# Performance work log

Hardware: AMD Instinct MI355X
Metric: run time of the kernel (lower is better)

The kernel has to match this reference:

```python
import jax, jax.numpy as jnp
import numpy as np

B, S, D, H, N, E = 4, 2048, 512, 8, 1024, 16384


def setup_inputs() -> dict:
    key = jax.random.key(0)
    ks = jax.random.split(key, 16)
    rn = lambda k, shp, s=0.02: jax.random.normal(k, shp, jnp.float32) * s
    x = jax.random.normal(ks[0], (B, S, D), jnp.float32)
    edge_index = jax.random.randint(ks[1], (2, E), 0, N)
    # unique sorted node positions per batch (equivalent to node_mask with N ones)
    node_indices = jnp.sort(
        jax.vmap(lambda k: jax.random.permutation(k, S)[:N])(jax.random.split(ks[2], B)),
        axis=1,
    )
    z = lambda shp: jnp.zeros(shp, jnp.float32)
    o = lambda shp: jnp.ones(shp, jnp.float32)
    return {
        "x": x,
        "edge_index": edge_index,
        "node_indices": node_indices,
        "Wq": rn(ks[3], (D, D)), "bq": z((D,)),
        "Wk": rn(ks[4], (D, D)), "bk": z((D,)),
        "Wv": rn(ks[5], (D, D)), "bv": z((D,)),
        "Wo": rn(ks[6], (D, D)), "bo": z((D,)),
        "Wf1": rn(ks[7], (D, 4 * D)), "bf1": z((4 * D,)),
        "Wf2": rn(ks[8], (4 * D, D)), "bf2": z((D,)),
        "g1": o((D,)), "be1": z((D,)),
        "g2": o((D,)), "be2": z((D,)),
        "g3": o((D,)), "be3": z((D,)),
        "Wg": rn(ks[9], (2 * D, D)), "bg": z((D,)),
        "Wgs": rn(ks[10], (D, D)), "Wgn": rn(ks[11], (D, D)), "bgn": z((D,)),
    }


def _ln(t, g, b, eps=1e-5):
    m = t.mean(-1, keepdims=True)
    v = ((t - m) ** 2).mean(-1, keepdims=True)
    return (t - m) * jax.lax.rsqrt(v + eps) * g + b


def reference(x, edge_index, node_indices, Wq, bq, Wk, bk, Wv, bv, Wo, bo,
              Wf1, bf1, Wf2, bf2, g1, be1, g2, be2, g3, be3, Wg, bg,
              Wgs, Wgn, bgn):
    Bs, Ss, Ds = x.shape
    Hn = H
    hd = Ds // Hn
    Nn = node_indices.shape[1]

    # --- self-attention (pre-norm, residual; dropout = eval identity) ---
    nx = _ln(x, g1, be1)
    q = (nx @ Wq + bq).reshape(Bs, Ss, Hn, hd).transpose(0, 2, 1, 3)
    k = (nx @ Wk + bk).reshape(Bs, Ss, Hn, hd).transpose(0, 2, 1, 3)
    v = (nx @ Wv + bv).reshape(Bs, Ss, Hn, hd).transpose(0, 2, 1, 3)
    scores = jnp.einsum('bhqd,bhkd->bhqk', q, k) / jnp.sqrt(jnp.float32(hd))
    attn = jax.nn.softmax(scores, axis=-1)
    ao = jnp.einsum('bhqk,bhkd->bhqd', attn, v).transpose(0, 2, 1, 3).reshape(Bs, Ss, Ds)
    x = x + ao @ Wo + bo

    # --- gather -> GNN -> scatter with sigmoid gate fusion ---
    nx2 = _ln(x, g2, be2)
    bidx = jnp.arange(Bs)[:, None]
    nodes = nx2[bidx, node_indices]                       # [B, N, D] gather
    src, dst = edge_index[0], edge_index[1]
    msgs = nodes[:, src, :]                               # [B, E, D]
    agg = jax.vmap(lambda m: jax.ops.segment_sum(m, dst, num_segments=Nn))(msgs)
    upd = jax.nn.relu(nodes @ Wgs + agg @ Wgn + bgn)      # GCN-like update
    gnn_out = jnp.zeros_like(nx2).at[bidx, node_indices].set(upd)  # scatter-back
    gate = jax.nn.sigmoid(jnp.concatenate([nx2, gnn_out], axis=-1) @ Wg + bg)
    x = x + gate * gnn_out + (1.0 - gate) * nx2

    # --- feed-forward ---
    nx3 = _ln(x, g3, be3)
    x = x + jax.nn.gelu(nx3 @ Wf1 + bf1, approximate=False) @ Wf2 + bf2
    return x
```

## Files before the change

### kernel.cpp

```cpp
#include <hip/hip_runtime.h>
#include <math.h>

using u16 = unsigned short;
using u32 = unsigned int;

typedef __attribute__((ext_vector_type(8))) short bf16x8;
typedef __attribute__((ext_vector_type(4))) float f32x4;

#define B_   4
#define S_   2048
#define D_   512
#define H_   8
#define HD_  64
#define N_   1024
#define E_   16384
#define DFF_ 2048
#define BS_  (B_ * S_)
#define BN_  (B_ * N_)
#define QSCALE 0.18033688011112042f
#define KSTRIDE 68
#define KSPLIT 2

__device__ __forceinline__ float bf2f(u16 u) {
  u32 v = (u32)u << 16; float f; __builtin_memcpy(&f, &v, 4); return f;
}
__device__ __forceinline__ u16 f2bf(float f) {
  u32 u; __builtin_memcpy(&u, &f, 4);
  u = u + 0x7fffu + ((u >> 16) & 1u);
  return (u16)(u >> 16);
}
__device__ __forceinline__ float bflo(u32 w) {
  u32 v = w << 16; float f; __builtin_memcpy(&f, &v, 4); return f;
}
__device__ __forceinline__ float bfhi(u32 w) {
  u32 v = w & 0xffff0000u; float f; __builtin_memcpy(&f, &v, 4); return f;
}
__device__ __forceinline__ u32 fbits(float f) { u32 u; __builtin_memcpy(&u, &f, 4); return u; }

__global__ __launch_bounds__(256) void tpose_all(const float* __restrict__ Wq, const float* __restrict__ Wk,
                                                 const float* __restrict__ Wv, const float* __restrict__ Wo,
                                                 const float* __restrict__ Wgs, const float* __restrict__ Wgn,
                                                 const float* __restrict__ Wg, const float* __restrict__ Wf1,
                                                 const float* __restrict__ Wf2, u16* __restrict__ wsbase) {
  __shared__ u16 t[32][33];
  const int z = blockIdx.z;
  const float* src; int C, r0, c0, ds, co; long doff;
  const long SL = 262144;
  switch (z) {
    case 0:  src = Wq;  C = 512;  r0 = 0;   c0 = 0;    ds = 512;  co = 0;   doff = 0;       break;
    case 1:  src = Wk;  C = 512;  r0 = 0;   c0 = 0;    ds = 512;  co = 0;   doff = 1 * SL;  break;
    case 2:  src = Wv;  C = 512;  r0 = 0;   c0 = 0;    ds = 512;  co = 0;   doff = 2 * SL;  break;
    case 3:  src = Wo;  C = 512;  r0 = 0;   c0 = 0;    ds = 512;  co = 0;   doff = 3 * SL;  break;
    case 4:  src = Wg;  C = 512;  r0 = 0;   c0 = 0;    ds = 1024; co = 0;   doff = 4 * SL;  break;
    case 5:  src = Wg;  C = 512;  r0 = 512; c0 = 0;    ds = 1024; co = 512; doff = 4 * SL;  break;
    case 6:  src = Wgs; C = 512;  r0 = 0;   c0 = 0;    ds = 1024; co = 0;   doff = 6 * SL;  break;
    case 7:  src = Wgn; C = 512;  r0 = 0;   c0 = 0;    ds = 1024; co = 512; doff = 6 * SL;  break;
    case 8: case 9: case 10: case 11:
             src = Wf1; C = 2048; r0 = 0;   c0 = (z - 8) * 512;  ds = 512;  co = 0; doff = 8 * SL;  break;
    default: src = Wf2; C = 512;  r0 = (z - 12) * 512; c0 = 0;   ds = 2048; co = (z - 12) * 512; doff = 12 * SL; break;
  }
  u16* dst = wsbase + doff;
  int rb = blockIdx.x * 32, cb = blockIdx.y * 32 + c0;
  int tx = threadIdx.x, ty = threadIdx.y;
  #pragma unroll
  for (int i = ty; i < 32; i += 8) t[i][tx] = f2bf(src[(long)(r0 + rb + i) * C + cb + tx]);
  __syncthreads();
  #pragma unroll
  for (int i = ty; i < 32; i += 8) dst[(long)(cb + i) * ds + co + rb + tx] = t[tx][i];
}

__global__ void packb_k(const float* __restrict__ bq, const float* __restrict__ bk,
                        const float* __restrict__ bv, float* __restrict__ o) {
  int i = blockIdx.x * 256 + threadIdx.x;
  if (i < 512) o[i] = bq[i];
  else if (i < 1024) o[i] = bk[i - 512];
  else if (i < 1536) o[i] = bv[i - 1024];
}

__global__ __launch_bounds__(256) void ln_k(const float* __restrict__ x, const float* __restrict__ g,
                                            const float* __restrict__ be, u16* __restrict__ out) {
  __shared__ float red[8];
  long row = blockIdx.x;
  int t = threadIdx.x;
  const float* xr = x + row * D_;
  float2 v = *(const float2*)(xr + 2 * t);
  float s = v.x + v.y, sq = v.x * v.x + v.y * v.y;
  #pragma unroll
  for (int m = 32; m >= 1; m >>= 1) { s += __shfl_xor(s, m, 64); sq += __shfl_xor(sq, m, 64); }
  if ((t & 63) == 0) { red[t >> 6] = s; red[4 + (t >> 6)] = sq; }
  __syncthreads();
  s = red[0] + red[1] + red[2] + red[3];
  sq = red[4] + red[5] + red[6] + red[7];
  float mean = s * (1.f / D_);
  float var = sq * (1.f / D_) - mean * mean;
  float rs = rsqrtf(fmaxf(var, 0.f) + 1e-5f);
  float2 gw = *(const float2*)(g + 2 * t);
  float2 bw = *(const float2*)(be + 2 * t);
  u32 o = (u32)f2bf((v.x - mean) * rs * gw.x + bw.x) | ((u32)f2bf((v.y - mean) * rs * gw.y + bw.y) << 16);
  *(u32*)&out[row * D_ + 2 * t] = o;
}

__device__ __forceinline__ void async_cp16(const u16* g, u16* l) {
  __builtin_amdgcn_global_load_lds((const __attribute__((address_space(1))) void*)g,
                                   (__attribute__((address_space(3))) void*)l, 16, 0, 0);
}

enum { EPI_QKV3, EPI_XF32, EPI_BF, EPI_RELU_SCATTER, EPI_GELU };

template <int EPI, bool CAT = false, int TM = 128>
__global__ __launch_bounds__(256) void gemm_k(const u16* __restrict__ A, const u16* __restrict__ A2,
                                              const u16* __restrict__ Bt, const float* __restrict__ bias,
                                              const void* src, void* out, const int* __restrict__ rowmap,
                                              int M, int N, int K) {
  constexpr int MT = (TM >= 32) ? (TM / 32) : 1;
  __shared__ __align__(16) u16 As[2 * TM * 32];
  __shared__ __align__(16) u16 Bs[8192];
  int tid = threadIdx.x;
  int lane = tid & 63;
  int wn = (tid >> 6) & 1;
  int wm = (tid >> 7) & 1;
  int nwg = gridDim.x * gridDim.y;
  int orig = blockIdx.y * gridDim.x + blockIdx.x;
  int wgid = ((orig & 7) * (nwg >> 3)) + (orig >> 3);
  int bx = wgid % gridDim.x;
  int by = wgid / gridDim.x;
  long m0 = (long)by * TM;
  long n0 = (long)bx * 128;

  f32x4 acc[MT][4];
  {
    f32x4 z = {0.f, 0.f, 0.f, 0.f};
    #pragma unroll
    for (int i = 0; i < MT; i++)
      #pragma unroll
      for (int j = 0; j < 4; j++) acc[i][j] = z;
  }

  int srow = tid >> 2;
  int skoff = (tid & 3) * 8;
  const int astride = CAT ? 512 : K;
  const u16* Ag  = A + (m0 + srow) * (long)astride + skoff;
  const u16* A2g = CAT ? (A2 + (m0 + srow) * (long)astride + skoff) : nullptr;
  const u16* Bg  = Bt + (n0 + srow) * (long)K + skoff;
  int rsel = lane & 15;
  int kchunk = (lane >> 4) * 8;

  for (int kt = 0; kt < K; kt += 64) {
    __syncthreads();
    #pragma unroll
    for (int s = 0; s < 2; s++) {
      int kts = kt + s * 32;
      const u16* Asrc = (CAT && kts >= 512) ? (A2g + (kts - 512)) : (Ag + kts);
      if constexpr (TM == 32) {
        if (tid < 128) async_cp16(Asrc, As + s * (TM * 32) + tid * 8);
      } else {
        async_cp16(Asrc, As + s * (TM * 32) + tid * 8);
        if constexpr (TM == 128) async_cp16(Asrc + (long)64 * astride, As + s * (TM * 32) + 2048 + tid * 8);
      }
      async_cp16(Bg + kts, Bs + s * 4096 + tid * 8);
      async_cp16(Bg + (long)64 * K + kts, Bs + s * 4096 + 2048 + tid * 8);
    }
    __syncthreads();
    #pragma unroll
    for (int s = 0; s < 2; s++) {
      bf16x8 af[MT], bfv[4];
      #pragma unroll
      for (int mt = 0; mt < MT; mt++)
        af[mt] = *(const bf16x8*)&As[s * (TM * 32) + (wm * (TM / 2) + mt * 16 + rsel) * 32 + kchunk];
      #pragma unroll
      for (int nt = 0; nt < 4; nt++)
        bfv[nt] = *(const bf16x8*)&Bs[s * 4096 + (wn * 64 + nt * 16 + rsel) * 32 + kchunk];
      #pragma unroll
      for (int mt = 0; mt < MT; mt++)
        #pragma unroll
        for (int nt = 0; nt < 4; nt++)
          acc[mt][nt] = __builtin_amdgcn_mfma_f32_16x16x32_bf16(af[mt], bfv[nt], acc[mt][nt], 0, 0, 0);
    }
  }

  int rbase = (lane >> 4) * 4;
  int cbase = lane & 15;
  #pragma unroll
  for (int mt = 0; mt < MT; mt++) {
    #pragma unroll
    for (int nt = 0; nt < 4; nt++) {
      long col = n0 + wn * 64 + nt * 16 + cbase;
      float bv = bias ? bias[col] : 0.f;
      long row0 = m0 + wm * (TM / 2) + mt * 16 + rbase;
      float vals[4];
      #pragma unroll
      for (int r = 0; r < 4; r++) vals[r] = acc[mt][nt][r] + bv;
      if constexpr (EPI == EPI_QKV3) {
        long which = col >> 9;
        long cc = col & 511;
        long b = row0 >> 11;
        long h = cc >> 6, d = cc & 63;
        if (which == 2) {
          long sI0 = row0 & 2047;
          uint2 w;
          w.x = (u32)f2bf(vals[0]) | ((u32)f2bf(vals[1]) << 16);
          w.y = (u32)f2bf(vals[2]) | ((u32)f2bf(vals[3]) << 16);
          *(uint2*)&((u16*)out)[2 * (long)BS_ * D_ + (((b * H_ + h) * HD_) + d) * S_ + sI0] = w;
        } else {
          #pragma unroll
          for (int r = 0; r < 4; r++) {
            long sI = (row0 + r) & 2047;
            float v2 = (which == 0) ? vals[r] * QSCALE : vals[r];
            ((u16*)out)[which * (long)BS_ * D_ + (((b * H_ + h) * S_) + sI) * HD_ + d] = f2bf(v2);
          }
        }
      } else {
        #pragma unroll
        for (int r = 0; r < 4; r++) {
          long row = row0 + r;
          float val = vals[r];
          if constexpr (EPI == EPI_XF32) {
            ((float*)out)[row * N + col] = val + ((const float*)src)[row * N + col];
          } else if constexpr (EPI == EPI_BF) {
            ((u16*)out)[row * N + col] = f2bf(val);
          } else if constexpr (EPI == EPI_RELU_SCATTER) {
            long orow = rowmap[row];
            ((u16*)out)[orow * D_ + col] = f2bf(fmaxf(val, 0.f));
          } else if constexpr (EPI == EPI_GELU) {
            ((u16*)out)[row * N + col] = f2bf(0.5f * val * (1.f + erff(val * 0.70710678118654752f)));
          }
        }
      }
    }
  }
}

__global__ __launch_bounds__(256) void attn_k(const u16* __restrict__ Q, const u16* __restrict__ Kv,
                                              const u16* __restrict__ VT, u16* __restrict__ Opart,
                                              float* __restrict__ Lp) {
  __shared__ __align__(16) u16 Ks[64 * KSTRIDE];
  __shared__ __align__(16) u16 Vs[64 * KSTRIDE];
  int tid = threadIdx.x;
  int lane = tid & 63;
  int wave = tid >> 6;
  int col = lane & 15;
  int quad = lane >> 4;
  int bh = blockIdx.y;
  int q0 = blockIdx.x * 128;
  int khalf = blockIdx.z;
  long base = (long)bh * S_;
  long vbase = (long)bh * HD_ * S_;

  const u16* qpa = Q + (base + q0 + wave * 32 + col) * HD_;
  const u16* qpb = qpa + 16 * HD_;
  bf16x8 bqa0 = *(const bf16x8*)(qpa + quad * 8);
  bf16x8 bqa1 = *(const bf16x8*)(qpa + 32 + quad * 8);
  bf16x8 bqb0 = *(const bf16x8*)(qpb + quad * 8);
  bf16x8 bqb1 = *(const bf16x8*)(qpb + 32 + quad * 8);

  float la = 0.f, lb = 0.f;
  f32x4 accA[4], accB[4];
  {
    f32x4 z = {0.f, 0.f, 0.f, 0.f};
    #pragma unroll
    for (int mt = 0; mt < 4; mt++) { accA[mt] = z; accB[mt] = z; }
  }

  int srow = tid >> 2;
  int sdc = (tid & 3) * 16;
  const bool hiQ = (quad >= 2);
  const int s0 = (quad & 1) * 2;
  const int a0 = (s0 * 16 + col + wave * 64) * 4;
  const int a1 = ((s0 + 1) * 16 + col + wave * 64) * 4;

  int kt0 = khalf * (S_ / KSPLIT);
  for (int kt = kt0; kt < kt0 + S_ / KSPLIT; kt += 64) {
    __syncthreads();
    {
      const u16* kg = Kv + (base + kt + srow) * HD_ + sdc;
      *(bf16x8*)&Ks[srow * KSTRIDE + sdc]     = *(const bf16x8*)kg;
      *(bf16x8*)&Ks[srow * KSTRIDE + sdc + 8] = *(const bf16x8*)(kg + 8);
      const u16* vg = VT + (vbase + (long)srow * S_) + kt + sdc;
      *(bf16x8*)&Vs[srow * KSTRIDE + sdc]     = *(const bf16x8*)vg;
      *(bf16x8*)&Vs[srow * KSTRIDE + sdc + 8] = *(const bf16x8*)(vg + 8);
    }
    __syncthreads();

    f32x4 sa[4], sb[4];
    #pragma unroll
    for (int nt = 0; nt < 4; nt++) {
      bf16x8 ak0 = *(const bf16x8*)&Ks[(nt * 16 + col) * KSTRIDE + quad * 8];
      bf16x8 ak1 = *(const bf16x8*)&Ks[(nt * 16 + col) * KSTRIDE + 32 + quad * 8];
      f32x4 z = {0.f, 0.f, 0.f, 0.f};
      z = __builtin_amdgcn_mfma_f32_16x16x32_bf16(ak0, bqa0, z, 0, 0, 0);
      z = __builtin_amdgcn_mfma_f32_16x16x32_bf16(ak1, bqa1, z, 0, 0, 0);
      sa[nt] = z;
      f32x4 y = {0.f, 0.f, 0.f, 0.f};
      y = __builtin_amdgcn_mfma_f32_16x16x32_bf16(ak0, bqb0, y, 0, 0, 0);
      y = __builtin_amdgcn_mfma_f32_16x16x32_bf16(ak1, bqb1, y, 0, 0, 0);
      sb[nt] = y;
    }

    u32 pka[4][2], pkb[4][2];
    #pragma unroll
    for (int nt = 0; nt < 4; nt++) {
      #pragma unroll
      for (int r = 0; r < 4; r++) { sa[nt][r] = __builtin_amdgcn_exp2f(sa[nt][r]); sb[nt][r] = __builtin_amdgcn_exp2f(sb[nt][r]); }
      la += (sa[nt][0] + sa[nt][1]) + (sa[nt][2] + sa[nt][3]);
      lb += (sb[nt][0] + sb[nt][1]) + (sb[nt][2] + sb[nt][3]);
      pka[nt][0] = __builtin_amdgcn_perm(fbits(sa[nt][1]), fbits(sa[nt][0]), 0x07060302u);
      pka[nt][1] = __builtin_amdgcn_perm(fbits(sa[nt][3]), fbits(sa[nt][2]), 0x07060302u);
      pkb[nt][0] = __builtin_amdgcn_perm(fbits(sb[nt][1]), fbits(sb[nt][0]), 0x07060302u);
      pkb[nt][1] = __builtin_amdgcn_perm(fbits(sb[nt][3]), fbits(sb[nt][2]), 0x07060302u);
    }

    union { u32 d[4]; bf16x8 v; } ba0, ba1, bb0, bb1;
    {
      u32 sA = hiQ ? pka[1][0] : pka[0][0];
      u32 sB = hiQ ? pka[1][1] : pka[0][1];
      ba0.d[0] = __builtin_amdgcn_ds_bpermute(a0, sA);
      ba0.d[1] = __builtin_amdgcn_ds_bpermute(a0, sB);
      ba0.d[2] = __builtin_amdgcn_ds_bpermute(a1, sA);
      ba0.d[3] = __builtin_amdgcn_ds_bpermute(a1, sB);
      u32 sC = hiQ ? pka[3][0] : pka[2][0];
      u32 sD = hiQ ? pka[3][1] : pka[2][1];
      ba1.d[0] = __builtin_amdgcn_ds_bpermute(a0, sC);
      ba1.d[1] = __builtin_amdgcn_ds_bpermute(a0, sD);
      ba1.d[2] = __builtin_amdgcn_ds_bpermute(a1, sC);
      ba1.d[3] = __builtin_amdgcn_ds_bpermute(a1, sD);
      u32 tA = hiQ ? pkb[1][0] : pkb[0][0];
      u32 tB = hiQ ? pkb[1][1] : pkb[0][1];
      bb0.d[0] = __builtin_amdgcn_ds_bpermute(a0, tA);
      bb0.d[1] = __builtin_amdgcn_ds_bpermute(a0, tB);
      bb0.d[2] = __builtin_amdgcn_ds_bpermute(a1, tA);
      bb0.d[3] = __builtin_amdgcn_ds_bpermute(a1, tB);
      u32 tC = hiQ ? pkb[3][0] : pkb[2][0];
      u32 tD = hiQ ? pkb[3][1] : pkb[2][1];
      bb1.d[0] = __builtin_amdgcn_ds_bpermute(a0, tC);
      bb1.d[1] = __builtin_amdgcn_ds_bpermute(a0, tD);
      bb1.d[2] = __builtin_amdgcn_ds_bpermute(a1, tC);
      bb1.d[3] = __builtin_amdgcn_ds_bpermute(a1, tD);
    }

    #pragma unroll
    for (int mt = 0; mt < 4; mt++) {
      bf16x8 av0 = *(const bf16x8*)&Vs[(mt * 16 + col) * KSTRIDE + quad * 8];
      bf16x8 av1 = *(const bf16x8*)&Vs[(mt * 16 + col) * KSTRIDE + 32 + quad * 8];
      accA[mt] = __builtin_amdgcn_mfma_f32_16x16x32_bf16(av0, ba0.v, accA[mt], 0, 0, 0);
      accA[mt] = __builtin_amdgcn_mfma_f32_16x16x32_bf16(av1, ba1.v, accA[mt], 0, 0, 0);
      accB[mt] = __builtin_amdgcn_mfma_f32_16x16x32_bf16(av0, bb0.v, accB[mt], 0, 0, 0);
      accB[mt] = __builtin_amdgcn_mfma_f32_16x16x32_bf16(av1, bb1.v, accB[mt], 0, 0, 0);
    }
  }

  la += __shfl_xor(la, 16, 64);
  la += __shfl_xor(la, 32, 64);
  lb += __shfl_xor(lb, 16, 64);
  lb += __shfl_xor(lb, 32, 64);

  int b = bh >> 3, h = bh & 7;
  long qrowA = (long)(b * S_) + q0 + wave * 32 + col;
  u16* Pp = Opart + (long)khalf * BS_ * D_;
  if (quad == 0) {
    float* lr = Lp + ((long)(khalf * 32 + bh)) * S_ + q0 + wave * 32;
    lr[col] = la;
    lr[16 + col] = lb;
  }
  u16* opA = Pp + qrowA * D_ + h * HD_ + quad * 4;
  u16* opB = Pp + (qrowA + 16) * D_ + h * HD_ + quad * 4;
  #pragma unroll
  for (int mt = 0; mt < 4; mt++) {
    uint2 w;
    w.x = (u32)f2bf(accA[mt][0]) | ((u32)f2bf(accA[mt][1]) << 16);
    w.y = (u32)f2bf(accA[mt][2]) | ((u32)f2bf(accA[mt][3]) << 16);
    *(uint2*)(opA + mt * 16) = w;
    uint2 v;
    v.x = (u32)f2bf(accB[mt][0]) | ((u32)f2bf(accB[mt][1]) << 16);
    v.y = (u32)f2bf(accB[mt][2]) | ((u32)f2bf(accB[mt][3]) << 16);
    *(uint2*)(opB + mt * 16) = v;
  }
}

__global__ __launch_bounds__(256) void acomb_k(const u16* __restrict__ P, const float* __restrict__ Lp,
                                               u16* __restrict__ AO) {
  long i = (long)blockIdx.x * 256 + threadIdx.x;
  long e0 = i * 4;
  long tok = e0 >> 9;
  int hh = (int)((e0 >> 6) & 7);
  long s = tok & 2047;
  long bb = tok >> 11;
  long bh = bb * 8 + hh;
  float l = 0.f;
  float v0 = 0.f, v1 = 0.f, v2 = 0.f, v3 = 0.f;
  #pragma unroll
  for (int k = 0; k < KSPLIT; k++) {
    uint2 a = ((const uint2*)(P + (long)k * BS_ * D_))[i];
    v0 += bflo(a.x); v1 += bfhi(a.x);
    v2 += bflo(a.y); v3 += bfhi(a.y);
    l += Lp[((long)(k * 32) + bh) * S_ + s];
  }
  float inv = 1.f / l;
  uint2 o;
  o.x = (u32)f2bf(v0 * inv) | ((u32)f2bf(v1 * inv) << 16);
  o.y = (u32)f2bf(v2 * inv) | ((u32)f2bf(v3 * inv) << 16);
  ((uint2*)AO)[i] = o;
}

__global__ __launch_bounds__(128) void gather_k(const u16* __restrict__ nx2, const int* __restrict__ nidx,
                                                int* __restrict__ rowmap, u16* __restrict__ Acat) {
  int bn = blockIdx.x;
  int t = threadIdx.x;
  long srow = (long)(bn >> 10) * S_ + nidx[bn];
  if (t == 0) rowmap[bn] = (int)srow;
  const u32* sp = (const u32*)(nx2 + srow * D_);
  u32* dp = (u32*)(Acat + (long)bn * 1024);
  dp[t] = sp[t];
  dp[t + 128] = sp[t + 128];
}

#define DEG_CAP 256
__global__ __launch_bounds__(256) void agg_k(const int* __restrict__ ei, u16* __restrict__ Acat) {
  __shared__ int cnt;
  __shared__ int lst[DEG_CAP];
  int n = blockIdx.x;
  int t = threadIdx.x;
  if (t == 0) cnt = 0;
  __syncthreads();
  const int* dst = ei + E_;
  for (int e = t; e < E_; e += 256) {
    if (dst[e] == n) {
      int idx = atomicAdd(&cnt, 1);
      if (idx < DEG_CAP) lst[idx] = ei[e];
    }
  }
  __syncthreads();
  int mcnt = cnt < DEG_CAP ? cnt : DEG_CAP;
  float2 acc[4] = {{0.f, 0.f}, {0.f, 0.f}, {0.f, 0.f}, {0.f, 0.f}};
  for (int i = 0; i < mcnt; i++) {
    long s = lst[i];
    #pragma unroll
    for (int b = 0; b < 4; b++) {
      u32 w = *(const u32*)&Acat[((long)(b * N_) + s) * 1024 + 2 * t];
      acc[b].x += bflo(w);
      acc[b].y += bfhi(w);
    }
  }
  #pragma unroll
  for (int b = 0; b < 4; b++) {
    u32 r = (u32)f2bf(acc[b].x) | ((u32)f2bf(acc[b].y) << 16);
    *(u32*)&Acat[((long)(b * N_) + n) * 1024 + 512 + 2 * t] = r;
  }
}

__global__ __launch_bounds__(256) void combln_k(const float* __restrict__ x1, const u16* __restrict__ gpre,
                                                const u16* __restrict__ gnn, const u16* __restrict__ nx2,
                                                const float* __restrict__ g3, const float* __restrict__ be3,
                                                float* __restrict__ x2, u16* __restrict__ nx3) {
  __shared__ float red[8];
  long row = blockIdx.x;
  int t = threadIdx.x;
  long off = row * D_ + 2 * t;
  float2 a = *(const float2*)(x1 + off);
  u32 gp = *(const u32*)(gpre + off);
  u32 gn = *(const u32*)(gnn + off);
  u32 nv = *(const u32*)(nx2 + off);
  float g0 = 1.f / (1.f + __expf(-bflo(gp)));
  float g1 = 1.f / (1.f + __expf(-bfhi(gp)));
  float t0 = a.x + g0 * bflo(gn) + (1.f - g0) * bflo(nv);
  float t1 = a.y + g1 * bfhi(gn) + (1.f - g1) * bfhi(nv);
  float2 w = {t0, t1};
  *(float2*)(x2 + off) = w;
  float s = t0 + t1, sq = t0 * t0 + t1 * t1;
  #pragma unroll
  for (int m = 32; m >= 1; m >>= 1) { s += __shfl_xor(s, m, 64); sq += __shfl_xor(sq, m, 64); }
  if ((t & 63) == 0) { red[t >> 6] = s; red[4 + (t >> 6)] = sq; }
  __syncthreads();
  s = red[0] + red[1] + red[2] + red[3];
  sq = red[4] + red[5] + red[6] + red[7];
  float mean = s * (1.f / D_);
  float var = sq * (1.f / D_) - mean * mean;
  float rs = rsqrtf(fmaxf(var, 0.f) + 1e-5f);
  float2 gw = *(const float2*)(g3 + 2 * t);
  float2 bw = *(const float2*)(be3 + 2 * t);
  u32 o = (u32)f2bf((t0 - mean) * rs * gw.x + bw.x) | ((u32)f2bf((t1 - mean) * rs * gw.y + bw.y) << 16);
  *(u32*)&nx3[off] = o;
}

extern "C" void kernel_launch(void* const* d_in, const int* in_sizes, int n_in,
                              void* d_out, int out_size, void* d_ws, size_t ws_size,
                              hipStream_t stream) {
  const float* x  = (const float*)d_in[0];
  const int* ei   = (const int*)d_in[1];
  const int* nidx = (const int*)d_in[2];
  const float* Wq = (const float*)d_in[3];   const float* bq = (const float*)d_in[4];
  const float* Wk = (const float*)d_in[5];   const float* bk = (const float*)d_in[6];
  const float* Wv = (const float*)d_in[7];   const float* bv = (const float*)d_in[8];
  const float* Wo = (const float*)d_in[9];   const float* bo = (const float*)d_in[10];
  const float* Wf1 = (const float*)d_in[11]; const float* bf1 = (const float*)d_in[12];
  const float* Wf2 = (const float*)d_in[13]; const float* bf2v = (const float*)d_in[14];
  const float* g1 = (const float*)d_in[15];  const float* be1 = (const float*)d_in[16];
  const float* g2 = (const float*)d_in[17];  const float* be2 = (const float*)d_in[18];
  const float* g3 = (const float*)d_in[19];  const float* be3 = (const float*)d_in[20];
  const float* Wg = (const float*)d_in[21];  const float* bg = (const float*)d_in[22];
  const float* Wgs = (const float*)d_in[23]; const float* Wgn = (const float*)d_in[24];
  const float* bgn = (const float*)d_in[25];

  const size_t MB8 = (size_t)8 * 1024 * 1024;
  char* base = (char*)d_ws;
  const size_t SLOT = (size_t)512 * 512 * 2;
  u16* WqT     = (u16*)(base + 0 * SLOT);
  u16* WoT     = (u16*)(base + 3 * SLOT);
  u16* WgFullT = (u16*)(base + 4 * SLOT);
  u16* WgsgnT  = (u16*)(base + 6 * SLOT);
  u16* Wf1T    = (u16*)(base + 8 * SLOT);
  u16* Wf2T    = (u16*)(base + 12 * SLOT);

  char* RA   = base + 16 * SLOT;
  char* Rqb  = RA + MB8;
  char* Rkb  = Rqb + MB8;
  char* Rvb  = Rkb + MB8;
  char* Rac  = Rvb + MB8;
  char* Rag  = Rac + MB8;
  char* Rx2  = Rag + MB8;
  char* RM   = Rx2 + 2 * MB8;

  u16* nx   = (u16*)RA;   u16* ao  = (u16*)RA;   u16* gnn = (u16*)RA;  u16* nx3 = (u16*)RA;
  u16* qb   = (u16*)Rqb;
  float* x1 = (float*)Rqb;
  u16* nx2  = (u16*)Rvb;
  u16* Opart = (u16*)Rac;
  u16* Acat = (u16*)Rac;
  u16* gpre = (u16*)Rac;
  float* x2 = (float*)Rx2;
  u16* ffh  = (u16*)Rqb;
  int* rowmap = (int*)RM;
  float* qkvb = (float*)(RM + 16384);
  float* Lpart = (float*)(RM + 32768);

  dim3 tb(32, 8);
  tpose_all<<<dim3(16, 16, 16), tb, 0, stream>>>(Wq, Wk, Wv, Wo, Wgs, Wgn, Wg, Wf1, Wf2, (u16*)base);
  packb_k<<<6, 256, 0, stream>>>(bq, bk, bv, qkvb);

  ln_k<<<BS_, 256, 0, stream>>>(x, g1, be1, nx);
  gemm_k<EPI_QKV3, false, 128><<<dim3(12, 64), 256, 0, stream>>>(nx, nullptr, WqT, qkvb, nullptr, qb, nullptr, BS_, 1536, 512);
  attn_k<<<dim3(S_ / 128, B_ * H_, KSPLIT), 256, 0, stream>>>(qb, qb + (long)BS_ * D_, qb + 2 * (long)BS_ * D_, Opart, Lpart);
  acomb_k<<<(BS_ * D_) / (256 * 4), 256, 0, stream>>>(Opart, Lpart, ao);
  gemm_k<EPI_XF32, false, 32><<<dim3(4, 256), 256, 0, stream>>>(ao, nullptr, WoT, bo, x, x1, nullptr, BS_, 512, 512);

  ln_k<<<BS_, 256, 0, stream>>>(x1, g2, be2, nx2);
  gather_k<<<BN_, 128, 0, stream>>>(nx2, nidx, rowmap, Acat);
  hipMemsetAsync(gnn, 0, (size_t)BS_ * D_ * 2, stream);
  agg_k<<<N_, 256, 0, stream>>>(ei, Acat);
  gemm_k<EPI_RELU_SCATTER, false, 32><<<dim3(4, 128), 256, 0, stream>>>(Acat, nullptr, WgsgnT, bgn, nullptr, gnn, rowmap, BN_, 512, 1024);

  gemm_k<EPI_BF, true, 32><<<dim3(4, 256), 256, 0, stream>>>(nx2, gnn, WgFullT, bg, nullptr, gpre, nullptr, BS_, 512, 1024);
  combln_k<<<BS_, 256, 0, stream>>>(x1, gpre, gnn, nx2, g3, be3, x2, nx3);

  gemm_k<EPI_GELU, false, 128><<<dim3(16, 64), 256, 0, stream>>>(nx3, nullptr, Wf1T, bf1, nullptr, ffh, nullptr, BS_, DFF_, 512);
  gemm_k<EPI_XF32, false, 32><<<dim3(4, 256), 256, 0, stream>>>(ffh, nullptr, Wf2T, bf2v, x2, (float*)d_out, nullptr, BS_, 512, DFF_);
}
```

Baseline: 399.3 us.

## Double-buffer GEMM K loop with prefetch; raise wave priority around attention MFMAs

The GEMM main loop now uses two 32-wide K buffers in shared memory. The next stage's async global-to-LDS copies are issued before the MFMAs on the current buffer, instead of loading both halves of a 64-wide tile and then computing. This aims to overlap memory loads with matrix math, at the cost of smaller per-iteration work and the same number of barriers per K. In the attention kernel, s_setprio(1) is wrapped around the QK and PV MFMA blocks so those waves get priority over the softmax and permute phases of other waves.

```diff
diff --git a/kernel.cpp b/kernel.cpp
--- a/kernel.cpp
+++ b/kernel.cpp
@@ -112,9 +112,9 @@
                                               const u16* __restrict__ Bt, const float* __restrict__ bias,
                                               const void* src, void* out, const int* __restrict__ rowmap,
                                               int M, int N, int K) {
-  constexpr int MT = (TM >= 32) ? (TM / 32) : 1;
-  __shared__ __align__(16) u16 As[2 * TM * 32];
-  __shared__ __align__(16) u16 Bs[8192];
+  constexpr int MT = TM / 32;
+  __shared__ __align__(16) u16 As[2][TM * 32];
+  __shared__ __align__(16) u16 Bs[2][4096];
   int tid = threadIdx.x;
   int lane = tid & 63;
   int wn = (tid >> 6) & 1;
@@ -145,37 +145,37 @@
   int rsel = lane & 15;
   int kchunk = (lane >> 4) * 8;
 
-  for (int kt = 0; kt < K; kt += 64) {
-    __syncthreads();
-    #pragma unroll
-    for (int s = 0; s < 2; s++) {
-      int kts = kt + s * 32;
-      const u16* Asrc = (CAT && kts >= 512) ? (A2g + (kts - 512)) : (Ag + kts);
-      if constexpr (TM == 32) {
-        if (tid < 128) async_cp16(Asrc, As + s * (TM * 32) + tid * 8);
-      } else {
-        async_cp16(Asrc, As + s * (TM * 32) + tid * 8);
-        if constexpr (TM == 128) async_cp16(Asrc + (long)64 * astride, As + s * (TM * 32) + 2048 + tid * 8);
-      }
-      async_cp16(Bg + kts, Bs + s * 4096 + tid * 8);
-      async_cp16(Bg + (long)64 * K + kts, Bs + s * 4096 + 2048 + tid * 8);
-    }
-    __syncthreads();
-    #pragma unroll
-    for (int s = 0; s < 2; s++) {
-      bf16x8 af[MT], bfv[4];
-      #pragma unroll
-      for (int mt = 0; mt < MT; mt++)
-        af[mt] = *(const bf16x8*)&As[s * (TM * 32) + (wm * (TM / 2) + mt * 16 + rsel) * 32 + kchunk];
+  auto stage = [&](int buf, int kts) {
+    const u16* Asrc = (CAT && kts >= 512) ? (A2g + (kts - 512)) : (Ag + kts);
+    if constexpr (TM == 32) {
+      if (tid < 128) async_cp16(Asrc, &As[buf][tid * 8]);
+    } else {
+      async_cp16(Asrc, &As[buf][tid * 8]);
+      if constexpr (TM == 128) async_cp16(Asrc + (long)64 * astride, &As[buf][2048 + tid * 8]);
+    }
+    async_cp16(Bg + kts, &Bs[buf][tid * 8]);
+    async_cp16(Bg + (long)64 * K + kts, &Bs[buf][2048 + tid * 8]);
+  };
+
+  stage(0, 0);
+  __syncthreads();
+  int buf = 0;
+  for (int kt = 0; kt < K; kt += 32) {
+    if (kt + 32 < K) stage(buf ^ 1, kt + 32);
+    bf16x8 af[MT], bfv[4];
+    #pragma unroll
+    for (int mt = 0; mt < MT; mt++)
+      af[mt] = *(const bf16x8*)&As[buf][(wm * (TM / 2) + mt * 16 + rsel) * 32 + kchunk];
+    #pragma unroll
+    for (int nt = 0; nt < 4; nt++)
+      bfv[nt] = *(const bf16x8*)&Bs[buf][(wn * 64 + nt * 16 + rsel) * 32 + kchunk];
+    #pragma unroll
+    for (int mt = 0; mt < MT; mt++)
       #pragma unroll
       for (int nt = 0; nt < 4; nt++)
-        bfv[nt] = *(const bf16x8*)&Bs[s * 4096 + (wn * 64 + nt * 16 + rsel) * 32 + kchunk];
-      #pragma unroll
-      for (int mt = 0; mt < MT; mt++)
-        #pragma unroll
-        for (int nt = 0; nt < 4; nt++)
-          acc[mt][nt] = __builtin_amdgcn_mfma_f32_16x16x32_bf16(af[mt], bfv[nt], acc[mt][nt], 0, 0, 0);
-    }
+        acc[mt][nt] = __builtin_amdgcn_mfma_f32_16x16x32_bf16(af[mt], bfv[nt], acc[mt][nt], 0, 0, 0);
+    __syncthreads();
+    buf ^= 1;
   }
 
   int rbase = (lane >> 4) * 4;
@@ -282,6 +282,7 @@
     __syncthreads();
 
     f32x4 sa[4], sb[4];
+    __builtin_amdgcn_s_setprio(1);
     #pragma unroll
     for (int nt = 0; nt < 4; nt++) {
       bf16x8 ak0 = *(const bf16x8*)&Ks[(nt * 16 + col) * KSTRIDE + quad * 8];
@@ -295,6 +296,7 @@
       y = __builtin_amdgcn_mfma_f32_16x16x32_bf16(ak1, bqb1, y, 0, 0, 0);
       sb[nt] = y;
     }
+    __builtin_amdgcn_s_setprio(0);
 
     u32 pka[4][2], pkb[4][2];
     #pragma unroll
@@ -337,6 +339,7 @@
       bb1.d[3] = __builtin_amdgcn_ds_bpermute(a1, tD);
     }
 
+    __builtin_amdgcn_s_setprio(1);
     #pragma unroll
     for (int mt = 0; mt < 4; mt++) {
       bf16x8 av0 = *(const bf16x8*)&Vs[(mt * 16 + col) * KSTRIDE + quad * 8];
@@ -346,6 +349,7 @@
       accB[mt] = __builtin_amdgcn_mfma_f32_16x16x32_bf16(av0, bb0.v, accB[mt], 0, 0, 0);
       accB[mt] = __builtin_amdgcn_mfma_f32_16x16x32_bf16(av1, bb1.v, accB[mt], 0, 0, 0);
     }
+    __builtin_amdgcn_s_setprio(0);
   }
 
   la += __shfl_xor(la, 16, 64);
```

Measured after the change: 417.5 us. +4.5%, slower.
